# Performance work log

Hardware: AMD Instinct MI355X
Metric: run time of the kernel (lower is better)

The kernel has to match this reference:

```python
import jax, jax.numpy as jnp
import numpy as np

H, DK, OUT, IN = 8, 64, 512, 512
N, E = 30000, 100000
SQRT_DK = float(np.sqrt(DK))


def _lin_params(k, din, dout):
    kw, = jax.random.split(k, 1)
    w = jax.random.normal(kw, (din, dout), jnp.float32) * (1.0 / np.sqrt(din))
    b = jnp.zeros((dout,), jnp.float32)
    return w, b


def setup_inputs() -> dict:
    key = jax.random.key(0)
    ks = jax.random.split(key, 24)
    inp = {
        'h_paper': jax.random.normal(ks[0], (N, IN), jnp.float32),
        'h_author': jax.random.normal(ks[1], (N, IN), jnp.float32),
        'src0': jax.random.randint(ks[2], (E,), 0, N),  # author ids
        'dst0': jax.random.randint(ks[3], (E,), 0, N),  # paper ids
        'src1': jax.random.randint(ks[4], (E,), 0, N),  # paper ids
        'dst1': jax.random.randint(ks[5], (E,), 0, N),  # author ids
    }
    # per-node-type linears (type 0 = paper, type 1 = author)
    i = 6
    for t in (0, 1):
        for nm in ('Wk', 'Wq', 'Wv', 'Wa'):
            w, b = _lin_params(ks[i], IN, OUT)
            inp[f'{nm}{t}'] = w
            inp[f'b{nm[1].lower()}{t}'] = b
            i += 1
    # relation parameters (xavier ~ uniform scaled; normal approx is fine for a reference)
    inp['rel_att'] = jax.random.normal(ks[22], (2, H, DK, DK), jnp.float32) * (1.0 / np.sqrt(DK))
    inp['rel_msg'] = jax.random.normal(ks[23], (2, H, DK, DK), jnp.float32) * (1.0 / np.sqrt(DK))
    inp['rel_pri'] = jnp.ones((2, H), jnp.float32)
    inp['skip'] = jnp.ones((2,), jnp.float32)
    return inp


def _relation_agg(h_src, Wk, bk, Wv, bv, h_dst, Wq, bq, src, dst, A, M, pri):
    # project src/dst node features to multi-head k/v/q: [N, H, DK]
    k = (h_src @ Wk + bk).reshape(-1, H, DK)
    v = (h_src @ Wv + bv).reshape(-1, H, DK)
    q = (h_dst @ Wq + bq).reshape(-1, H, DK)
    # per-edge relation-specific transforms (HGT Step 1/2)
    key_e = jnp.einsum('ehk,hkd->ehd', k[src], A)   # [E,H,DK]
    val_e = jnp.einsum('ehk,hkd->ehd', v[src], M)   # [E,H,DK]
    att = (q[dst] * key_e).sum(-1) * pri / SQRT_DK  # [E,H]
    # segment softmax over incoming edges of each destination node
    m = jax.ops.segment_max(att, dst, num_segments=N)
    m = jnp.where(jnp.isfinite(m), m, 0.0)
    e = jnp.exp(att - m[dst])
    s = jax.ops.segment_sum(e, dst, num_segments=N)
    a = e / s[dst]                                   # [E,H]
    t = jax.ops.segment_sum(a[..., None] * val_e, dst, num_segments=N)
    return t.reshape(N, OUT)


def reference(h_paper, h_author, src0, dst0, src1, dst1,
              Wk0, bk0, Wq0, bq0, Wv0, bv0, Wa0, ba0,
              Wk1, bk1, Wq1, bq1, Wv1, bv1, Wa1, ba1,
              rel_att, rel_msg, rel_pri, skip):
    # relation 0: author (type 1) -> paper (type 0)
    t_paper = _relation_agg(h_author, Wk1, bk1, Wv1, bv1, h_paper, Wq0, bq0,
                            src0, dst0, rel_att[0], rel_msg[0], rel_pri[0])
    # relation 1: paper (type 0) -> author (type 1)
    t_author = _relation_agg(h_paper, Wk0, bk0, Wv0, bv0, h_author, Wq1, bq1,
                             src1, dst1, rel_att[1], rel_msg[1], rel_pri[1])
    # Step 3: target-specific aggregation with sigmoid skip (dropout=0 -> identity)
    a0 = jax.nn.sigmoid(skip[0])
    a1 = jax.nn.sigmoid(skip[1])
    out_paper = (t_paper @ Wa0 + ba0) * a0 + h_paper * (1.0 - a0)
    out_author = (t_author @ Wa1 + ba1) * a1 + h_author * (1.0 - a1)
    return jnp.stack([out_paper, out_author])  # [2, N, OUT]
```

## Files before the change

kernel.cpp:

```cpp
#include <hip/hip_runtime.h>
#include <hip/hip_bf16.h>
#include <stdint.h>

#define N_NODES 30000
#define N_PAD   30080
#define N_EDGES 100000
#define DIM     512
#define QKV_LD  1536

typedef unsigned short ushort_t;
typedef __attribute__((ext_vector_type(8))) short short8;
typedef __attribute__((ext_vector_type(8))) unsigned short ushortx8;
typedef __attribute__((ext_vector_type(4))) float floatx4;

__device__ __forceinline__ float b2f(ushort_t b) { return __uint_as_float(((unsigned)b) << 16); }
__device__ __forceinline__ ushort_t f2b(float f) {
    unsigned u = __float_as_uint(f);
    u += 0x7FFFu + ((u >> 16) & 1u);
    return (ushort_t)(u >> 16);
}

__global__ __launch_bounds__(256) void pad_copy2(const float* __restrict__ h0,
                                                 const float* __restrict__ h1,
                                                 ushort_t* __restrict__ d0,
                                                 ushort_t* __restrict__ d1) {
    const int total = N_PAD * DIM / 4;
    const int valid = N_NODES * DIM / 4;
    int idx = blockIdx.x * 256 + threadIdx.x;
    if (idx >= total) return;
    const float* s = blockIdx.y ? h1 : h0;
    ushort_t* d = blockIdx.y ? d1 : d0;
    float4 v = make_float4(0.f, 0.f, 0.f, 0.f);
    if (idx < valid) v = ((const float4*)s)[idx];
    ushort_t o[4] = {f2b(v.x), f2b(v.y), f2b(v.z), f2b(v.w)};
    ((uint2*)d)[idx] = *(const uint2*)o;
}

__global__ __launch_bounds__(256) void fuse_weights4(const float* __restrict__ Wk0, const float* __restrict__ bk0,
                                                     const float* __restrict__ Wv0, const float* __restrict__ bv0,
                                                     const float* __restrict__ Wk1, const float* __restrict__ bk1,
                                                     const float* __restrict__ Wv1, const float* __restrict__ bv1,
                                                     const float* __restrict__ rel_att, const float* __restrict__ rel_msg,
                                                     ushort_t* __restrict__ cat_p, ushort_t* __restrict__ cat_a,
                                                     float* __restrict__ bias_p, float* __restrict__ bias_a) {
    const float *W, *bvec, *A;
    ushort_t* outw; float* outb;
    switch (blockIdx.y) {
        case 0: W = Wk1; bvec = bk1; A = rel_att;          outw = cat_a + 512 * DIM;  outb = bias_a + 512;  break;
        case 1: W = Wv1; bvec = bv1; A = rel_msg;          outw = cat_a + 1024 * DIM; outb = bias_a + 1024; break;
        case 2: W = Wk0; bvec = bk0; A = rel_att + 32768;  outw = cat_p + 512 * DIM;  outb = bias_p + 512;  break;
        default: W = Wv0; bvec = bv0; A = rel_msg + 32768; outw = cat_p + 1024 * DIM; outb = bias_p + 1024; break;
    }
    int idx = blockIdx.x * 256 + threadIdx.x;
    int n = idx & 511;
    int i = idx >> 9;
    int h = n >> 6, d = n & 63;
    const float* wrow = W + i * DIM + h * 64;
    const float* acol = A + h * 4096 + d;
    float s = 0.f;
#pragma unroll 8
    for (int c = 0; c < 64; ++c) s += wrow[c] * acol[c * 64];
    outw[n * DIM + i] = f2b(s);
    if (i == 0) {
        const float* bh = bvec + h * 64;
        float sb = 0.f;
        for (int c = 0; c < 64; ++c) sb += bh[c] * acol[c * 64];
        outb[n] = sb;
    }
}

__global__ __launch_bounds__(256) void transpose4(const float* w0, const float* w1,
                                                  const float* w2, const float* w3,
                                                  ushort_t* o0, ushort_t* o1,
                                                  ushort_t* o2, ushort_t* o3) {
    const float* W; ushort_t* O;
    switch (blockIdx.y) {
        case 0: W = w0; O = o0; break;
        case 1: W = w1; O = o1; break;
        case 2: W = w2; O = o2; break;
        default: W = w3; O = o3; break;
    }
    __shared__ float tile[32][33];
    int bx = blockIdx.x & 15, by = blockIdx.x >> 4;
    int tx = threadIdx.x & 31, ty = threadIdx.x >> 5;
#pragma unroll
    for (int r = 0; r < 32; r += 8) tile[ty + r][tx] = W[(by * 32 + ty + r) * DIM + bx * 32 + tx];
    __syncthreads();
#pragma unroll
    for (int r = 0; r < 32; r += 8) O[(bx * 32 + ty + r) * DIM + by * 32 + tx] = f2b(tile[tx][ty + r]);
}

__global__ __launch_bounds__(256) void copy_biases(const float* bq0, const float* bq1,
                                                   float* bias_p, float* bias_a) {
    int i = blockIdx.x * 256 + threadIdx.x;
    bias_p[i] = bq0[i];
    bias_a[i] = bq1[i];
}

__global__ __launch_bounds__(256) void hist2(const int* __restrict__ dst0, const int* __restrict__ dst1,
                                             int* __restrict__ cnt) {
    int e = blockIdx.x * 256 + threadIdx.x;
    if (e >= 2 * N_EDGES) return;
    int rel = e >= N_EDGES;
    int d = (rel ? dst1 : dst0)[e - rel * N_EDGES];
    atomicAdd(&cnt[rel * N_NODES + d], 1);
}

__global__ __launch_bounds__(1024) void scan2(const int* __restrict__ cnt, int* __restrict__ row_ptr) {
    int rel = blockIdx.x;
    const int* c = cnt + rel * N_NODES;
    int* rp = row_ptr + rel * (N_NODES + 1);
    __shared__ int sums[1024];
    int tid = threadIdx.x;
    int base = tid * 32;
    int loc[32];
    int s = 0;
#pragma unroll
    for (int i = 0; i < 32; ++i) {
        int idx = base + i;
        int v = (idx < N_NODES) ? c[idx] : 0;
        s += v;
        loc[i] = s;
    }
    sums[tid] = s;
    __syncthreads();
    for (int off = 1; off < 1024; off <<= 1) {
        int add = (tid >= off) ? sums[tid - off] : 0;
        __syncthreads();
        sums[tid] += add;
        __syncthreads();
    }
    int pre = (tid > 0) ? sums[tid - 1] : 0;
    if (tid == 0) rp[0] = 0;
#pragma unroll
    for (int i = 0; i < 32; ++i) {
        int idx = base + i;
        if (idx < N_NODES) rp[idx + 1] = pre + loc[i];
    }
}

__global__ __launch_bounds__(256) void scatter2(const int* __restrict__ src0, const int* __restrict__ dst0,
                                                const int* __restrict__ src1, const int* __restrict__ dst1,
                                                const int* __restrict__ row_ptr,
                                                int* __restrict__ fill,
                                                int* __restrict__ colarr) {
    int e = blockIdx.x * 256 + threadIdx.x;
    if (e >= 2 * N_EDGES) return;
    int rel = e >= N_EDGES;
    int ei = e - rel * N_EDGES;
    int s = (rel ? src1 : src0)[ei];
    int d = (rel ? dst1 : dst0)[ei];
    int pos = atomicAdd(&fill[rel * N_NODES + d], 1);
    colarr[rel * N_EDGES + row_ptr[rel * (N_NODES + 1) + d] + pos] = s;
}

typedef const __attribute__((address_space(1))) unsigned int gu32;
typedef __attribute__((address_space(3))) unsigned int lu32;
__device__ __forceinline__ void gload_lds16(const void* g, void* l) {
    __builtin_amdgcn_global_load_lds((gu32*)g, (lu32*)l, 16, 0, 0);
}

__global__ __launch_bounds__(256) void gemm_proj(const ushort_t* __restrict__ Ap, const ushort_t* __restrict__ Aa,
                                                 const ushort_t* __restrict__ Bp, const ushort_t* __restrict__ Ba,
                                                 const float* __restrict__ bias_p, const float* __restrict__ bias_a,
                                                 ushort_t* __restrict__ Cp, ushort_t* __restrict__ Ca) {
    int rel = blockIdx.z;
    const ushort_t* A = rel ? Aa : Ap;
    const ushort_t* BT = rel ? Ba : Bp;
    const float* bias = rel ? bias_a : bias_p;
    ushort_t* C = rel ? Ca : Cp;

    __shared__ alignas(16) ushort_t As[128 * 32];
    __shared__ alignas(16) ushort_t Bs[128 * 32];
    int n0 = blockIdx.x * 128, m0 = blockIdx.y * 128;
    int tid = threadIdx.x;
    int w = tid >> 6, l = tid & 63;
    int wr = w >> 1, wc = w & 1;
    int fr = l & 15, fq = l >> 4;
    floatx4 acc[4][4] = {};
    const ushort_t* aF = &As[(wr * 64 + fr) * 32 + fq * 8];
    const ushort_t* bF = &Bs[(wc * 64 + fr) * 32 + fq * 8];
    int row0 = tid >> 2, c0 = (tid & 3) * 8;
    int row1 = (tid + 256) >> 2;
    int lb0 = (w * 64) * 16;
    int lb1 = (256 + w * 64) * 16;

#pragma unroll 1
    for (int kt = 0; kt < 16; ++kt) {
        int k0 = kt * 32;
        if (kt) __syncthreads();
        gload_lds16(A + (size_t)(m0 + row0) * DIM + k0 + c0, (char*)As + lb0);
        gload_lds16(BT + (size_t)(n0 + row0) * DIM + k0 + c0, (char*)Bs + lb0);
        gload_lds16(A + (size_t)(m0 + row1) * DIM + k0 + c0, (char*)As + lb1);
        gload_lds16(BT + (size_t)(n0 + row1) * DIM + k0 + c0, (char*)Bs + lb1);
        __syncthreads();
        short8 af[4], bf[4];
#pragma unroll
        for (int i = 0; i < 4; ++i) af[i] = *(const short8*)(aF + i * 16 * 32);
#pragma unroll
        for (int j = 0; j < 4; ++j) bf[j] = *(const short8*)(bF + j * 16 * 32);
#pragma unroll
        for (int i = 0; i < 4; ++i)
#pragma unroll
            for (int j = 0; j < 4; ++j)
                acc[i][j] = __builtin_amdgcn_mfma_f32_16x16x32_bf16(af[i], bf[j], acc[i][j], 0, 0, 0);
    }
#pragma unroll
    for (int i = 0; i < 4; ++i)
#pragma unroll
        for (int j = 0; j < 4; ++j) {
            int col = n0 + wc * 64 + j * 16 + fr;
            float bc = bias[col];
#pragma unroll
            for (int r = 0; r < 4; ++r) {
                int grow = m0 + wr * 64 + i * 16 + fq * 4 + r;
                C[(size_t)grow * QKV_LD + col] = f2b(acc[i][j][r] + bc);
            }
        }
}

__global__ __launch_bounds__(256) void gemm_out(const ushort_t* __restrict__ Tp, const ushort_t* __restrict__ Ta,
                                                const ushort_t* __restrict__ Wp, const ushort_t* __restrict__ Wa,
                                                const float* __restrict__ ba0, const float* __restrict__ ba1,
                                                const float* __restrict__ hp, const float* __restrict__ ha,
                                                const float* __restrict__ skipv, float* __restrict__ out) {
    int rel = blockIdx.z;
    const ushort_t* A = rel ? Ta : Tp;
    const ushort_t* BT = rel ? Wa : Wp;
    const float* bias = rel ? ba1 : ba0;
    const float* Hres = rel ? ha : hp;
    float* C = out + (size_t)rel * N_NODES * DIM;

    __shared__ alignas(16) ushort_t As[128 * 32];
    __shared__ alignas(16) ushort_t Bs[128 * 32];
    int n0 = blockIdx.x * 128, m0 = blockIdx.y * 128;
    int tid = threadIdx.x;
    int w = tid >> 6, l = tid & 63;
    int wr = w >> 1, wc = w & 1;
    int fr = l & 15, fq = l >> 4;
    floatx4 acc[4][4] = {};
    const ushort_t* aF = &As[(wr * 64 + fr) * 32 + fq * 8];
    const ushort_t* bF = &Bs[(wc * 64 + fr) * 32 + fq * 8];
    int row0 = tid >> 2, c0 = (tid & 3) * 8;
    int row1 = (tid + 256) >> 2;
    int lb0 = (w * 64) * 16;
    int lb1 = (256 + w * 64) * 16;

#pragma unroll 1
    for (int kt = 0; kt < 16; ++kt) {
        int k0 = kt * 32;
        if (kt) __syncthreads();
        gload_lds16(A + (size_t)(m0 + row0) * QKV_LD + k0 + c0, (char*)As + lb0);
        gload_lds16(BT + (size_t)(n0 + row0) * DIM + k0 + c0, (char*)Bs + lb0);
        gload_lds16(A + (size_t)(m0 + row1) * QKV_LD + k0 + c0, (char*)As + lb1);
        gload_lds16(BT + (size_t)(n0 + row1) * DIM + k0 + c0, (char*)Bs + lb1);
        __syncthreads();
        short8 af[4], bf[4];
#pragma unroll
        for (int i = 0; i < 4; ++i) af[i] = *(const short8*)(aF + i * 16 * 32);
#pragma unroll
        for (int j = 0; j < 4; ++j) bf[j] = *(const short8*)(bF + j * 16 * 32);
#pragma unroll
        for (int i = 0; i < 4; ++i)
#pragma unroll
            for (int j = 0; j < 4; ++j)
                acc[i][j] = __builtin_amdgcn_mfma_f32_16x16x32_bf16(af[i], bf[j], acc[i][j], 0, 0, 0);
    }
    float sk = skipv[rel];
    float alpha = 1.f / (1.f + __expf(-sk));
    float onem = 1.f - alpha;
#pragma unroll
    for (int i = 0; i < 4; ++i)
#pragma unroll
        for (int j = 0; j < 4; ++j) {
            int col = n0 + wc * 64 + j * 16 + fr;
            float bc = bias[col];
#pragma unroll
            for (int r = 0; r < 4; ++r) {
                int grow = m0 + wr * 64 + i * 16 + fq * 4 + r;
                if (grow < N_NODES) {
                    float v = acc[i][j][r] + bc;
                    C[(size_t)grow * DIM + col] = v * alpha + Hres[(size_t)grow * DIM + col] * onem;
                }
            }
        }
}

__global__ __launch_bounds__(256) void node_attn(const ushort_t* __restrict__ qkv_p,
                                                 ushort_t* __restrict__ qkv_p_mut,
                                                 const ushort_t* __restrict__ qkv_a,
                                                 ushort_t* __restrict__ qkv_a_mut,
                                                 const int* __restrict__ row_ptr,
                                                 const int* __restrict__ colarr,
                                                 const float* __restrict__ rel_pri) {
    int rel = blockIdx.y;
    const ushort_t* qkv_dst = rel ? qkv_a : qkv_p;
    ushort_t* t_out = rel ? qkv_a_mut : qkv_p_mut;
    const ushort_t* qkv_src = rel ? qkv_p : qkv_a;
    const int* rp = row_ptr + rel * (N_NODES + 1);
    const int* col = colarr + rel * N_EDGES;
    const float* pri = rel_pri + rel * 8;

    int w = threadIdx.x >> 6, l = threadIdx.x & 63;
    int n = blockIdx.x * 4 + w;
    float prih = pri[l >> 3] * 0.125f;

    size_t qoff = (size_t)n * QKV_LD + l * 8;
    ushortx8 qr = *(const ushortx8*)(qkv_dst + qoff);
    float qd[8];
#pragma unroll
    for (int i = 0; i < 8; ++i) qd[i] = b2f(qr[i]);

    int lo = 0, hi = 0;
    if (n < N_NODES) { lo = rp[n]; hi = rp[n + 1]; }

    float m = -3.0e38f, s = 0.f;
    float acc[8] = {};
    int j = lo;
    ushortx8 kr, vr;
    if (j < hi) {
        int sn = col[j];
        const ushort_t* kb = qkv_src + (size_t)sn * QKV_LD + 512 + l * 8;
        kr = *(const ushortx8*)kb;
        vr = *(const ushortx8*)(kb + 512);
    }
    while (j < hi) {
        ushortx8 kc = kr, vc = vr;
        ++j;
        if (j < hi) {
            int sn = col[j];
            const ushort_t* kb = qkv_src + (size_t)sn * QKV_LD + 512 + l * 8;
            kr = *(const ushortx8*)kb;
            vr = *(const ushortx8*)(kb + 512);
        }
        float dot = 0.f;
#pragma unroll
        for (int i = 0; i < 8; ++i) dot += qd[i] * b2f(kc[i]);
        dot += __shfl_xor(dot, 1);
        dot += __shfl_xor(dot, 2);
        dot += __shfl_xor(dot, 4);
        float att = dot * prih;
        float mn = fmaxf(m, att);
        float e0 = __expf(m - mn);
        float e1 = __expf(att - mn);
        s = s * e0 + e1;
#pragma unroll
        for (int i = 0; i < 8; ++i) acc[i] = acc[i] * e0 + e1 * b2f(vc[i]);
        m = mn;
    }
    float inv = (hi > lo) ? 1.f / s : 0.f;
    ushortx8 o;
#pragma unroll
    for (int i = 0; i < 8; ++i) o[i] = f2b(acc[i] * inv);
    *(ushortx8*)(t_out + qoff) = o;
}

extern "C" void kernel_launch(void* const* d_in, const int* in_sizes, int n_in,
                              void* d_out, int out_size, void* d_ws, size_t ws_size,
                              hipStream_t stream) {
    (void)in_sizes; (void)n_in; (void)out_size; (void)ws_size;
    const float* h_paper  = (const float*)d_in[0];
    const float* h_author = (const float*)d_in[1];
    const int* src0 = (const int*)d_in[2];
    const int* dst0 = (const int*)d_in[3];
    const int* src1 = (const int*)d_in[4];
    const int* dst1 = (const int*)d_in[5];
    const float* Wk0 = (const float*)d_in[6];  const float* bk0 = (const float*)d_in[7];
    const float* Wq0 = (const float*)d_in[8];  const float* bq0 = (const float*)d_in[9];
    const float* Wv0 = (const float*)d_in[10]; const float* bv0 = (const float*)d_in[11];
    const float* Wa0 = (const float*)d_in[12]; const float* ba0 = (const float*)d_in[13];
    const float* Wk1 = (const float*)d_in[14]; const float* bk1 = (const float*)d_in[15];
    const float* Wq1 = (const float*)d_in[16]; const float* bq1 = (const float*)d_in[17];
    const float* Wv1 = (const float*)d_in[18]; const float* bv1 = (const float*)d_in[19];
    const float* Wa1 = (const float*)d_in[20]; const float* ba1 = (const float*)d_in[21];
    const float* rel_att = (const float*)d_in[22];
    const float* rel_msg = (const float*)d_in[23];
    const float* rel_pri = (const float*)d_in[24];
    const float* skipv   = (const float*)d_in[25];
    float* out = (float*)d_out;

    char* p = (char*)d_ws;
    auto alloc = [&](size_t bytes) -> char* {
        char* r = p;
        p += (bytes + 255) & ~(size_t)255;
        return r;
    };
    ushort_t* hp_pad = (ushort_t*)alloc((size_t)N_PAD * DIM * 2);
    ushort_t* ha_pad = (ushort_t*)alloc((size_t)N_PAD * DIM * 2);
    ushort_t* qkv_p = (ushort_t*)alloc((size_t)N_PAD * QKV_LD * 2);
    ushort_t* qkv_a = (ushort_t*)alloc((size_t)N_PAD * QKV_LD * 2);
    ushort_t* cat_p = (ushort_t*)alloc((size_t)QKV_LD * DIM * 2);
    ushort_t* cat_a = (ushort_t*)alloc((size_t)QKV_LD * DIM * 2);
    ushort_t* WaT0 = (ushort_t*)alloc(DIM * DIM * 2);
    ushort_t* WaT1 = (ushort_t*)alloc(DIM * DIM * 2);
    float* bias_p = (float*)alloc(QKV_LD * 4);
    float* bias_a = (float*)alloc(QKV_LD * 4);
    int* cnt = (int*)alloc((size_t)4 * N_NODES * 4);
    int* fill = cnt + 2 * N_NODES;
    int* row_ptr = (int*)alloc((size_t)2 * (N_NODES + 1) * 4);
    int* colarr = (int*)alloc((size_t)2 * N_EDGES * 4);

    pad_copy2<<<dim3((N_PAD * DIM / 4 + 255) / 256, 2), 256, 0, stream>>>(h_paper, h_author, hp_pad, ha_pad);
    fuse_weights4<<<dim3(1024, 4), 256, 0, stream>>>(Wk0, bk0, Wv0, bv0, Wk1, bk1, Wv1, bv1,
                                                     rel_att, rel_msg, cat_p, cat_a, bias_p, bias_a);
    transpose4<<<dim3(256, 4), 256, 0, stream>>>(Wq0, Wq1, Wa0, Wa1, cat_p, cat_a, WaT0, WaT1);
    copy_biases<<<2, 256, 0, stream>>>(bq0, bq1, bias_p, bias_a);

    hipMemsetAsync(cnt, 0, (size_t)4 * N_NODES * 4, stream);
    hist2<<<(2 * N_EDGES + 255) / 256, 256, 0, stream>>>(dst0, dst1, cnt);
    scan2<<<2, 1024, 0, stream>>>(cnt, row_ptr);
    scatter2<<<(2 * N_EDGES + 255) / 256, 256, 0, stream>>>(src0, dst0, src1, dst1, row_ptr, fill, colarr);

    gemm_proj<<<dim3(12, 235, 2), 256, 0, stream>>>(hp_pad, ha_pad, cat_p, cat_a, bias_p, bias_a, qkv_p, qkv_a);

    node_attn<<<dim3(N_PAD / 4, 2), 256, 0, stream>>>(qkv_p, qkv_p, qkv_a, qkv_a, row_ptr, colarr, rel_pri);

    gemm_out<<<dim3(4, 235, 2), 256, 0, stream>>>(qkv_p, qkv_a, WaT0, WaT1, ba0, ba1,
                                                  h_paper, h_author, skipv, out);
}
```

Before: 692.5 us.

## Double-buffer LDS tiles in projection and output GEMMs to prefetch next K-slice

Both bf16 MFMA GEMM kernels now keep two LDS buffers per operand. Each iteration issues the global-to-LDS async loads for the next K-slice before computing on the current one, which removes one barrier per iteration and hides global load latency behind the MFMA work. Row offsets are precomputed outside the loop. The cost is twice the LDS per block (32 KB instead of 16 KB), which may lower occupancy.

```diff
diff --git a/kernel.cpp b/kernel.cpp
--- a/kernel.cpp
+++ b/kernel.cpp
@@ -170,30 +170,41 @@
     const float* bias = rel ? bias_a : bias_p;
     ushort_t* C = rel ? Ca : Cp;
 
-    __shared__ alignas(16) ushort_t As[128 * 32];
-    __shared__ alignas(16) ushort_t Bs[128 * 32];
+    __shared__ alignas(16) ushort_t As[2][128 * 32];
+    __shared__ alignas(16) ushort_t Bs[2][128 * 32];
     int n0 = blockIdx.x * 128, m0 = blockIdx.y * 128;
     int tid = threadIdx.x;
     int w = tid >> 6, l = tid & 63;
     int wr = w >> 1, wc = w & 1;
     int fr = l & 15, fq = l >> 4;
     floatx4 acc[4][4] = {};
-    const ushort_t* aF = &As[(wr * 64 + fr) * 32 + fq * 8];
-    const ushort_t* bF = &Bs[(wc * 64 + fr) * 32 + fq * 8];
     int row0 = tid >> 2, c0 = (tid & 3) * 8;
-    int row1 = (tid + 256) >> 2;
+    int row1 = row0 + 64;
     int lb0 = (w * 64) * 16;
     int lb1 = (256 + w * 64) * 16;
-
+    const size_t a0 = (size_t)(m0 + row0) * DIM + c0;
+    const size_t a1 = (size_t)(m0 + row1) * DIM + c0;
+    const size_t b0 = (size_t)(n0 + row0) * DIM + c0;
+    const size_t b1 = (size_t)(n0 + row1) * DIM + c0;
+
+    gload_lds16(A + a0, (char*)As[0] + lb0);
+    gload_lds16(BT + b0, (char*)Bs[0] + lb0);
+    gload_lds16(A + a1, (char*)As[0] + lb1);
+    gload_lds16(BT + b1, (char*)Bs[0] + lb1);
+
+    int cur = 0;
 #pragma unroll 1
     for (int kt = 0; kt < 16; ++kt) {
-        int k0 = kt * 32;
-        if (kt) __syncthreads();
-        gload_lds16(A + (size_t)(m0 + row0) * DIM + k0 + c0, (char*)As + lb0);
-        gload_lds16(BT + (size_t)(n0 + row0) * DIM + k0 + c0, (char*)Bs + lb0);
-        gload_lds16(A + (size_t)(m0 + row1) * DIM + k0 + c0, (char*)As + lb1);
-        gload_lds16(BT + (size_t)(n0 + row1) * DIM + k0 + c0, (char*)Bs + lb1);
         __syncthreads();
+        if (kt < 15) {
+            int k0 = (kt + 1) * 32;
+            gload_lds16(A + a0 + k0, (char*)As[cur ^ 1] + lb0);
+            gload_lds16(BT + b0 + k0, (char*)Bs[cur ^ 1] + lb0);
+            gload_lds16(A + a1 + k0, (char*)As[cur ^ 1] + lb1);
+            gload_lds16(BT + b1 + k0, (char*)Bs[cur ^ 1] + lb1);
+        }
+        const ushort_t* aF = &As[cur][(wr * 64 + fr) * 32 + fq * 8];
+        const ushort_t* bF = &Bs[cur][(wc * 64 + fr) * 32 + fq * 8];
         short8 af[4], bf[4];
 #pragma unroll
         for (int i = 0; i < 4; ++i) af[i] = *(const short8*)(aF + i * 16 * 32);
@@ -204,6 +215,7 @@
 #pragma unroll
             for (int j = 0; j < 4; ++j)
                 acc[i][j] = __builtin_amdgcn_mfma_f32_16x16x32_bf16(af[i], bf[j], acc[i][j], 0, 0, 0);
+        cur ^= 1;
     }
 #pragma unroll
     for (int i = 0; i < 4; ++i)
@@ -231,30 +243,41 @@
     const float* Hres = rel ? ha : hp;
     float* C = out + (size_t)rel * N_NODES * DIM;
 
-    __shared__ alignas(16) ushort_t As[128 * 32];
-    __shared__ alignas(16) ushort_t Bs[128 * 32];
+    __shared__ alignas(16) ushort_t As[2][128 * 32];
+    __shared__ alignas(16) ushort_t Bs[2][128 * 32];
     int n0 = blockIdx.x * 128, m0 = blockIdx.y * 128;
     int tid = threadIdx.x;
     int w = tid >> 6, l = tid & 63;
     int wr = w >> 1, wc = w & 1;
     int fr = l & 15, fq = l >> 4;
     floatx4 acc[4][4] = {};
-    const ushort_t* aF = &As[(wr * 64 + fr) * 32 + fq * 8];
-    const ushort_t* bF = &Bs[(wc * 64 + fr) * 32 + fq * 8];
     int row0 = tid >> 2, c0 = (tid & 3) * 8;
-    int row1 = (tid + 256) >> 2;
+    int row1 = row0 + 64;
     int lb0 = (w * 64) * 16;
     int lb1 = (256 + w * 64) * 16;
-
+    const size_t a0 = (size_t)(m0 + row0) * QKV_LD + c0;
+    const size_t a1 = (size_t)(m0 + row1) * QKV_LD + c0;
+    const size_t b0 = (size_t)(n0 + row0) * DIM + c0;
+    const size_t b1 = (size_t)(n0 + row1) * DIM + c0;
+
+    gload_lds16(A + a0, (char*)As[0] + lb0);
+    gload_lds16(BT + b0, (char*)Bs[0] + lb0);
+    gload_lds16(A + a1, (char*)As[0] + lb1);
+    gload_lds16(BT + b1, (char*)Bs[0] + lb1);
+
+    int cur = 0;
 #pragma unroll 1
     for (int kt = 0; kt < 16; ++kt) {
-        int k0 = kt * 32;
-        if (kt) __syncthreads();
-        gload_lds16(A + (size_t)(m0 + row0) * QKV_LD + k0 + c0, (char*)As + lb0);
-        gload_lds16(BT + (size_t)(n0 + row0) * DIM + k0 + c0, (char*)Bs + lb0);
-        gload_lds16(A + (size_t)(m0 + row1) * QKV_LD + k0 + c0, (char*)As + lb1);
-        gload_lds16(BT + (size_t)(n0 + row1) * DIM + k0 + c0, (char*)Bs + lb1);
         __syncthreads();
+        if (kt < 15) {
+            int k0 = (kt + 1) * 32;
+            gload_lds16(A + a0 + k0, (char*)As[cur ^ 1] + lb0);
+            gload_lds16(BT + b0 + k0, (char*)Bs[cur ^ 1] + lb0);
+            gload_lds16(A + a1 + k0, (char*)As[cur ^ 1] + lb1);
+            gload_lds16(BT + b1 + k0, (char*)Bs[cur ^ 1] + lb1);
+        }
+        const ushort_t* aF = &As[cur][(wr * 64 + fr) * 32 + fq * 8];
+        const ushort_t* bF = &Bs[cur][(wc * 64 + fr) * 32 + fq * 8];
         short8 af[4], bf[4];
 #pragma unroll
         for (int i = 0; i < 4; ++i) af[i] = *(const short8*)(aF + i * 16 * 32);
@@ -265,6 +288,7 @@
 #pragma unroll
             for (int j = 0; j < 4; ++j)
                 acc[i][j] = __builtin_amdgcn_mfma_f32_16x16x32_bf16(af[i], bf[j], acc[i][j], 0, 0, 0);
+        cur ^= 1;
     }
     float sk = skipv[rel];
     float alpha = 1.f / (1.f + __expf(-sk));
```

After: 690.0 us. No clear change (-0.4%).

## Restructure projection and output GEMMs to keep full A row-panel in LDS

Applied to the files above, without the earlier changes.

Both GEMMs now load a 64-row by full-K panel of A into padded LDS once per block, then each wave streams its own 128-column slice of B directly from global memory into registers, with no per-k-step LDS staging or barriers. The projection kernel loops over three 512-column chunks so one block covers all of QKV for its rows, and the grid becomes one block per 64-row tile per relation. This removes repeated A reloads and the per-iteration synchronisation. In exchange, B is read from global or L2 without LDS sharing, there are more accumulator registers per wave, and a large LDS footprint may reduce occupancy.

```diff
diff --git a/kernel.cpp b/kernel.cpp
--- a/kernel.cpp
+++ b/kernel.cpp
@@ -7,6 +7,7 @@
 #define N_EDGES 100000
 #define DIM     512
 #define QKV_LD  1536
+#define A_LDS_W 520
 
 typedef unsigned short ushort_t;
 typedef __attribute__((ext_vector_type(8))) short short8;
@@ -164,59 +165,57 @@
                                                  const ushort_t* __restrict__ Bp, const ushort_t* __restrict__ Ba,
                                                  const float* __restrict__ bias_p, const float* __restrict__ bias_a,
                                                  ushort_t* __restrict__ Cp, ushort_t* __restrict__ Ca) {
-    int rel = blockIdx.z;
+    int rel = blockIdx.y;
     const ushort_t* A = rel ? Aa : Ap;
     const ushort_t* BT = rel ? Ba : Bp;
     const float* bias = rel ? bias_a : bias_p;
     ushort_t* C = rel ? Ca : Cp;
 
-    __shared__ alignas(16) ushort_t As[128 * 32];
-    __shared__ alignas(16) ushort_t Bs[128 * 32];
-    int n0 = blockIdx.x * 128, m0 = blockIdx.y * 128;
+    __shared__ alignas(16) ushort_t As[64 * A_LDS_W];
+    int m0 = blockIdx.x * 64;
     int tid = threadIdx.x;
     int w = tid >> 6, l = tid & 63;
-    int wr = w >> 1, wc = w & 1;
+#pragma unroll
+    for (int t = 0; t < 16; ++t) {
+        int r = w * 16 + t;
+        gload_lds16(A + (size_t)(m0 + r) * DIM + l * 8, (char*)As + r * (A_LDS_W * 2));
+    }
     int fr = l & 15, fq = l >> 4;
-    floatx4 acc[4][4] = {};
-    const ushort_t* aF = &As[(wr * 64 + fr) * 32 + fq * 8];
-    const ushort_t* bF = &Bs[(wc * 64 + fr) * 32 + fq * 8];
-    int row0 = tid >> 2, c0 = (tid & 3) * 8;
-    int row1 = (tid + 256) >> 2;
-    int lb0 = (w * 64) * 16;
-    int lb1 = (256 + w * 64) * 16;
+    const ushort_t* aF = As + fr * A_LDS_W + fq * 8;
+    const ushort_t* Bw0 = BT + (size_t)(w * 128 + fr) * DIM + fq * 8;
+    __syncthreads();
 
 #pragma unroll 1
-    for (int kt = 0; kt < 16; ++kt) {
-        int k0 = kt * 32;
-        if (kt) __syncthreads();
-        gload_lds16(A + (size_t)(m0 + row0) * DIM + k0 + c0, (char*)As + lb0);
-        gload_lds16(BT + (size_t)(n0 + row0) * DIM + k0 + c0, (char*)Bs + lb0);
-        gload_lds16(A + (size_t)(m0 + row1) * DIM + k0 + c0, (char*)As + lb1);
-        gload_lds16(BT + (size_t)(n0 + row1) * DIM + k0 + c0, (char*)Bs + lb1);
-        __syncthreads();
-        short8 af[4], bf[4];
-#pragma unroll
-        for (int i = 0; i < 4; ++i) af[i] = *(const short8*)(aF + i * 16 * 32);
-#pragma unroll
-        for (int j = 0; j < 4; ++j) bf[j] = *(const short8*)(bF + j * 16 * 32);
-#pragma unroll
-        for (int i = 0; i < 4; ++i)
-#pragma unroll
-            for (int j = 0; j < 4; ++j)
-                acc[i][j] = __builtin_amdgcn_mfma_f32_16x16x32_bf16(af[i], bf[j], acc[i][j], 0, 0, 0);
-    }
-#pragma unroll
-    for (int i = 0; i < 4; ++i)
-#pragma unroll
-        for (int j = 0; j < 4; ++j) {
-            int col = n0 + wc * 64 + j * 16 + fr;
-            float bc = bias[col];
-#pragma unroll
-            for (int r = 0; r < 4; ++r) {
-                int grow = m0 + wr * 64 + i * 16 + fq * 4 + r;
-                C[(size_t)grow * QKV_LD + col] = f2b(acc[i][j][r] + bc);
+    for (int c = 0; c < 3; ++c) {
+        const ushort_t* Bw = Bw0 + (size_t)c * 512 * DIM;
+        floatx4 acc[4][8] = {};
+#pragma unroll 1
+        for (int kt = 0; kt < 16; ++kt) {
+            int k0 = kt * 32;
+            short8 bf[8], af[4];
+#pragma unroll
+            for (int nj = 0; nj < 8; ++nj) bf[nj] = *(const short8*)(Bw + (size_t)nj * 16 * DIM + k0);
+#pragma unroll
+            for (int mi = 0; mi < 4; ++mi) af[mi] = *(const short8*)(aF + mi * 16 * A_LDS_W + k0);
+#pragma unroll
+            for (int mi = 0; mi < 4; ++mi)
+#pragma unroll
+                for (int nj = 0; nj < 8; ++nj)
+                    acc[mi][nj] = __builtin_amdgcn_mfma_f32_16x16x32_bf16(af[mi], bf[nj], acc[mi][nj], 0, 0, 0);
+        }
+#pragma unroll
+        for (int mi = 0; mi < 4; ++mi)
+#pragma unroll
+            for (int nj = 0; nj < 8; ++nj) {
+                int col = c * 512 + w * 128 + nj * 16 + fr;
+                float bc = bias[col];
+#pragma unroll
+                for (int r = 0; r < 4; ++r) {
+                    int grow = m0 + mi * 16 + fq * 4 + r;
+                    C[(size_t)grow * QKV_LD + col] = f2b(acc[mi][nj][r] + bc);
+                }
             }
-        }
+    }
 }
 
 __global__ __launch_bounds__(256) void gemm_out(const ushort_t* __restrict__ Tp, const ushort_t* __restrict__ Ta,
@@ -224,62 +223,56 @@
                                                 const float* __restrict__ ba0, const float* __restrict__ ba1,
                                                 const float* __restrict__ hp, const float* __restrict__ ha,
                                                 const float* __restrict__ skipv, float* __restrict__ out) {
-    int rel = blockIdx.z;
+    int rel = blockIdx.y;
     const ushort_t* A = rel ? Ta : Tp;
     const ushort_t* BT = rel ? Wa : Wp;
     const float* bias = rel ? ba1 : ba0;
     const float* Hres = rel ? ha : hp;
     float* C = out + (size_t)rel * N_NODES * DIM;
 
-    __shared__ alignas(16) ushort_t As[128 * 32];
-    __shared__ alignas(16) ushort_t Bs[128 * 32];
-    int n0 = blockIdx.x * 128, m0 = blockIdx.y * 128;
+    __shared__ alignas(16) ushort_t As[64 * A_LDS_W];
+    int m0 = blockIdx.x * 64;
     int tid = threadIdx.x;
     int w = tid >> 6, l = tid & 63;
-    int wr = w >> 1, wc = w & 1;
+#pragma unroll
+    for (int t = 0; t < 16; ++t) {
+        int r = w * 16 + t;
+        gload_lds16(A + (size_t)(m0 + r) * QKV_LD + l * 8, (char*)As + r * (A_LDS_W * 2));
+    }
     int fr = l & 15, fq = l >> 4;
-    floatx4 acc[4][4] = {};
-    const ushort_t* aF = &As[(wr * 64 + fr) * 32 + fq * 8];
-    const ushort_t* bF = &Bs[(wc * 64 + fr) * 32 + fq * 8];
-    int row0 = tid >> 2, c0 = (tid & 3) * 8;
-    int row1 = (tid + 256) >> 2;
-    int lb0 = (w * 64) * 16;
-    int lb1 = (256 + w * 64) * 16;
-
+    const ushort_t* aF = As + fr * A_LDS_W + fq * 8;
+    const ushort_t* Bw = BT + (size_t)(w * 128 + fr) * DIM + fq * 8;
+    __syncthreads();
+
+    floatx4 acc[4][8] = {};
 #pragma unroll 1
     for (int kt = 0; kt < 16; ++kt) {
         int k0 = kt * 32;
-        if (kt) __syncthreads();
-        gload_lds16(A + (size_t)(m0 + row0) * QKV_LD + k0 + c0, (char*)As + lb0);
-        gload_lds16(BT + (size_t)(n0 + row0) * DIM + k0 + c0, (char*)Bs + lb0);
-        gload_lds16(A + (size_t)(m0 + row1) * QKV_LD + k0 + c0, (char*)As + lb1);
-        gload_lds16(BT + (size_t)(n0 + row1) * DIM + k0 + c0, (char*)Bs + lb1);
-        __syncthreads();
-        short8 af[4], bf[4];
-#pragma unroll
-        for (int i = 0; i < 4; ++i) af[i] = *(const short8*)(aF + i * 16 * 32);
-#pragma unroll
-        for (int j = 0; j < 4; ++j) bf[j] = *(const short8*)(bF + j * 16 * 32);
-#pragma unroll
-        for (int i = 0; i < 4; ++i)
-#pragma unroll
-            for (int j = 0; j < 4; ++j)
-                acc[i][j] = __builtin_amdgcn_mfma_f32_16x16x32_bf16(af[i], bf[j], acc[i][j], 0, 0, 0);
+        short8 bf[8], af[4];
+#pragma unroll
+        for (int nj = 0; nj < 8; ++nj) bf[nj] = *(const short8*)(Bw + (size_t)nj * 16 * DIM + k0);
+#pragma unroll
+        for (int mi = 0; mi < 4; ++mi) af[mi] = *(const short8*)(aF + mi * 16 * A_LDS_W + k0);
+#pragma unroll
+        for (int mi = 0; mi < 4; ++mi)
+#pragma unroll
+            for (int nj = 0; nj < 8; ++nj)
+                acc[mi][nj] = __builtin_amdgcn_mfma_f32_16x16x32_bf16(af[mi], bf[nj], acc[mi][nj], 0, 0, 0);
     }
     float sk = skipv[rel];
     float alpha = 1.f / (1.f + __expf(-sk));
     float onem = 1.f - alpha;
 #pragma unroll
-    for (int i = 0; i < 4; ++i)
-#pragma unroll
-        for (int j = 0; j < 4; ++j) {
-            int col = n0 + wc * 64 + j * 16 + fr;
+    for (int mi = 0; mi < 4; ++mi)
+#pragma unroll
+        for (int nj = 0; nj < 8; ++nj) {
+            int col = w * 128 + nj * 16 + fr;
             float bc = bias[col];
 #pragma unroll
             for (int r = 0; r < 4; ++r) {
-                int grow = m0 + wr * 64 + i * 16 + fq * 4 + r;
+                int grow = m0 + mi * 16 + fq * 4 + r;
                 if (grow < N_NODES) {
-                    float v = acc[i][j][r] + bc;
+                    float v = acc[mi][nj][r] + bc;
                     C[(size_t)grow * DIM + col] = v * alpha + Hres[(size_t)grow * DIM + col] * onem;
                 }
             }
@@ -411,10 +404,10 @@
     scan2<<<2, 1024, 0, stream>>>(cnt, row_ptr);
     scatter2<<<(2 * N_EDGES + 255) / 256, 256, 0, stream>>>(src0, dst0, src1, dst1, row_ptr, fill, colarr);
 
-    gemm_proj<<<dim3(12, 235, 2), 256, 0, stream>>>(hp_pad, ha_pad, cat_p, cat_a, bias_p, bias_a, qkv_p, qkv_a);
+    gemm_proj<<<dim3(N_PAD / 64, 2), 256, 0, stream>>>(hp_pad, ha_pad, cat_p, cat_a, bias_p, bias_a, qkv_p, qkv_a);
 
     node_attn<<<dim3(N_PAD / 4, 2), 256, 0, stream>>>(qkv_p, qkv_p, qkv_a, qkv_a, row_ptr, colarr, rel_pri);
 
-    gemm_out<<<dim3(4, 235, 2), 256, 0, stream>>>(qkv_p, qkv_a, WaT0, WaT1, ba0, ba1,
-                                                  h_paper, h_author, skipv, out);
-}
+    gemm_out<<<dim3(N_PAD / 64, 2), 256, 0, stream>>>(qkv_p, qkv_a, WaT0, WaT1, ba0, ba1,
+                                                      h_paper, h_author, skipv, out);
+}
```

Result: slower. 914.0 us (+32.0%).

## Use 8-wave GEMM blocks with XCD-aware linear block remapping

Applied to the files above, without the earlier changes.

Both GEMM kernels now launch 512-thread blocks (8 waves) per 128x128 tile, each wave computing a 32x64 sub-tile instead of 64x64. Half the threads stage A and half stage B, one 16-byte async load each per 64-row half. Blocks use a 1D grid remapped so consecutive blocks on the same XCD (bid&7) cover adjacent tiles, which is meant to improve L2 reuse and latency hiding. The cost is fewer accumulators per wave, so each wave does less MFMA work per LDS fragment load.

```diff
diff --git a/kernel.cpp b/kernel.cpp
--- a/kernel.cpp
+++ b/kernel.cpp
@@ -160,11 +160,15 @@
     __builtin_amdgcn_global_load_lds((gu32*)g, (lu32*)l, 16, 0, 0);
 }
 
-__global__ __launch_bounds__(256) void gemm_proj(const ushort_t* __restrict__ Ap, const ushort_t* __restrict__ Aa,
+__global__ __launch_bounds__(512) void gemm_proj(const ushort_t* __restrict__ Ap, const ushort_t* __restrict__ Aa,
                                                  const ushort_t* __restrict__ Bp, const ushort_t* __restrict__ Ba,
                                                  const float* __restrict__ bias_p, const float* __restrict__ bias_a,
                                                  ushort_t* __restrict__ Cp, ushort_t* __restrict__ Ca) {
-    int rel = blockIdx.z;
+    int bid = blockIdx.x;
+    int lin = (bid & 7) * 705 + (bid >> 3);
+    int rel = lin >= 2820;
+    int r = lin - rel * 2820;
+    int my = r / 12, nx = r - my * 12;
     const ushort_t* A = rel ? Aa : Ap;
     const ushort_t* BT = rel ? Ba : Bp;
     const float* bias = rel ? bias_a : bias_p;
@@ -172,59 +176,63 @@
 
     __shared__ alignas(16) ushort_t As[128 * 32];
     __shared__ alignas(16) ushort_t Bs[128 * 32];
-    int n0 = blockIdx.x * 128, m0 = blockIdx.y * 128;
+    int n0 = nx * 128, m0 = my * 128;
     int tid = threadIdx.x;
     int w = tid >> 6, l = tid & 63;
     int wr = w >> 1, wc = w & 1;
     int fr = l & 15, fq = l >> 4;
-    floatx4 acc[4][4] = {};
-    const ushort_t* aF = &As[(wr * 64 + fr) * 32 + fq * 8];
+    floatx4 acc[2][4] = {};
+    const ushort_t* aF = &As[(wr * 32 + fr) * 32 + fq * 8];
     const ushort_t* bF = &Bs[(wc * 64 + fr) * 32 + fq * 8];
-    int row0 = tid >> 2, c0 = (tid & 3) * 8;
-    int row1 = (tid + 256) >> 2;
-    int lb0 = (w * 64) * 16;
-    int lb1 = (256 + w * 64) * 16;
+    int g = tid & 255;
+    int srow = g >> 2, sc0 = (g & 3) * 8;
+    const ushort_t* gsrc0 = (tid < 256) ? (A + (size_t)(m0 + srow) * DIM + sc0)
+                                        : (BT + (size_t)(n0 + srow) * DIM + sc0);
+    const ushort_t* gsrc1 = gsrc0 + (size_t)64 * DIM;
+    char* ldst = (tid < 256) ? ((char*)As + g * 16) : ((char*)Bs + g * 16);
 
 #pragma unroll 1
     for (int kt = 0; kt < 16; ++kt) {
         int k0 = kt * 32;
         if (kt) __syncthreads();
-        gload_lds16(A + (size_t)(m0 + row0) * DIM + k0 + c0, (char*)As + lb0);
-        gload_lds16(BT + (size_t)(n0 + row0) * DIM + k0 + c0, (char*)Bs + lb0);
-        gload_lds16(A + (size_t)(m0 + row1) * DIM + k0 + c0, (char*)As + lb1);
-        gload_lds16(BT + (size_t)(n0 + row1) * DIM + k0 + c0, (char*)Bs + lb1);
+        gload_lds16(gsrc0 + k0, ldst);
+        gload_lds16(gsrc1 + k0, ldst + 4096);
         __syncthreads();
-        short8 af[4], bf[4];
-#pragma unroll
-        for (int i = 0; i < 4; ++i) af[i] = *(const short8*)(aF + i * 16 * 32);
+        short8 af[2], bf[4];
+#pragma unroll
+        for (int i = 0; i < 2; ++i) af[i] = *(const short8*)(aF + i * 16 * 32);
 #pragma unroll
         for (int j = 0; j < 4; ++j) bf[j] = *(const short8*)(bF + j * 16 * 32);
 #pragma unroll
-        for (int i = 0; i < 4; ++i)
+        for (int i = 0; i < 2; ++i)
 #pragma unroll
             for (int j = 0; j < 4; ++j)
                 acc[i][j] = __builtin_amdgcn_mfma_f32_16x16x32_bf16(af[i], bf[j], acc[i][j], 0, 0, 0);
     }
 #pragma unroll
-    for (int i = 0; i < 4; ++i)
+    for (int i = 0; i < 2; ++i)
 #pragma unroll
         for (int j = 0; j < 4; ++j) {
             int col = n0 + wc * 64 + j * 16 + fr;
             float bc = bias[col];
 #pragma unroll
-            for (int r = 0; r < 4; ++r) {
-                int grow = m0 + wr * 64 + i * 16 + fq * 4 + r;
-                C[(size_t)grow * QKV_LD + col] = f2b(acc[i][j][r] + bc);
+            for (int rr = 0; rr < 4; ++rr) {
+                int grow = m0 + wr * 32 + i * 16 + fq * 4 + rr;
+                C[(size_t)grow * QKV_LD + col] = f2b(acc[i][j][rr] + bc);
             }
         }
 }
 
-__global__ __launch_bounds__(256) void gemm_out(const ushort_t* __restrict__ Tp, const ushort_t* __restrict__ Ta,
+__global__ __launch_bounds__(512) void gemm_out(const ushort_t* __restrict__ Tp, const ushort_t* __restrict__ Ta,
                                                 const ushort_t* __restrict__ Wp, const ushort_t* __restrict__ Wa,
                                                 const float* __restrict__ ba0, const float* __restrict__ ba1,
                                                 const float* __restrict__ hp, const float* __restrict__ ha,
                                                 const float* __restrict__ skipv, float* __restrict__ out) {
-    int rel = blockIdx.z;
+    int bid = blockIdx.x;
+    int lin = (bid & 7) * 235 + (bid >> 3);
+    int rel = lin >= 940;
+    int r = lin - rel * 940;
+    int my = r >> 2, nx = r & 3;
     const ushort_t* A = rel ? Ta : Tp;
     const ushort_t* BT = rel ? Wa : Wp;
     const float* bias = rel ? ba1 : ba0;
@@ -233,35 +241,35 @@
 
     __shared__ alignas(16) ushort_t As[128 * 32];
     __shared__ alignas(16) ushort_t Bs[128 * 32];
-    int n0 = blockIdx.x * 128, m0 = blockIdx.y * 128;
+    int n0 = nx * 128, m0 = my * 128;
     int tid = threadIdx.x;
     int w = tid >> 6, l = tid & 63;
     int wr = w >> 1, wc = w & 1;
     int fr = l & 15, fq = l >> 4;
-    floatx4 acc[4][4] = {};
-    const ushort_t* aF = &As[(wr * 64 + fr) * 32 + fq * 8];
+    floatx4 acc[2][4] = {};
+    const ushort_t* aF = &As[(wr * 32 + fr) * 32 + fq * 8];
     const ushort_t* bF = &Bs[(wc * 64 + fr) * 32 + fq * 8];
-    int row0 = tid >> 2, c0 = (tid & 3) * 8;
-    int row1 = (tid + 256) >> 2;
-    int lb0 = (w * 64) * 16;
-    int lb1 = (256 + w * 64) * 16;
+    int g = tid & 255;
+    int srow = g >> 2, sc0 = (g & 3) * 8;
+    const ushort_t* gsrc0 = (tid < 256) ? (A + (size_t)(m0 + srow) * QKV_LD + sc0)
+                                        : (BT + (size_t)(n0 + srow) * DIM + sc0);
+    const ushort_t* gsrc1 = gsrc0 + (size_t)64 * ((tid < 256) ? QKV_LD : DIM);
+    char* ldst = (tid < 256) ? ((char*)As + g * 16) : ((char*)Bs + g * 16);
 
 #pragma unroll 1
     for (int kt = 0; kt < 16; ++kt) {
         int k0 = kt * 32;
         if (kt) __syncthreads();
-        gload_lds16(A + (size_t)(m0 + row0) * QKV_LD + k0 + c0, (char*)As + lb0);
-        gload_lds16(BT + (size_t)(n0 + row0) * DIM + k0 + c0, (char*)Bs + lb0);
-        gload_lds16(A + (size_t)(m0 + row1) * QKV_LD + k0 + c0, (char*)As + lb1);
-        gload_lds16(BT + (size_t)(n0 + row1) * DIM + k0 + c0, (char*)Bs + lb1);
+        gload_lds16(gsrc0 + k0, ldst);
+        gload_lds16(gsrc1 + k0, ldst + 4096);
         __syncthreads();
-        short8 af[4], bf[4];
-#pragma unroll
-        for (int i = 0; i < 4; ++i) af[i] = *(const short8*)(aF + i * 16 * 32);
+        short8 af[2], bf[4];
+#pragma unroll
+        for (int i = 0; i < 2; ++i) af[i] = *(const short8*)(aF + i * 16 * 32);
 #pragma unroll
         for (int j = 0; j < 4; ++j) bf[j] = *(const short8*)(bF + j * 16 * 32);
 #pragma unroll
-        for (int i = 0; i < 4; ++i)
+        for (int i = 0; i < 2; ++i)
 #pragma unroll
             for (int j = 0; j < 4; ++j)
                 acc[i][j] = __builtin_amdgcn_mfma_f32_16x16x32_bf16(af[i], bf[j], acc[i][j], 0, 0, 0);
@@ -270,16 +278,16 @@
     float alpha = 1.f / (1.f + __expf(-sk));
     float onem = 1.f - alpha;
 #pragma unroll
-    for (int i = 0; i < 4; ++i)
+    for (int i = 0; i < 2; ++i)
 #pragma unroll
         for (int j = 0; j < 4; ++j) {
             int col = n0 + wc * 64 + j * 16 + fr;
             float bc = bias[col];
 #pragma unroll
-            for (int r = 0; r < 4; ++r) {
-                int grow = m0 + wr * 64 + i * 16 + fq * 4 + r;
+            for (int rr = 0; rr < 4; ++rr) {
+                int grow = m0 + wr * 32 + i * 16 + fq * 4 + rr;
                 if (grow < N_NODES) {
-                    float v = acc[i][j][r] + bc;
+                    float v = acc[i][j][rr] + bc;
                     C[(size_t)grow * DIM + col] = v * alpha + Hres[(size_t)grow * DIM + col] * onem;
                 }
             }
@@ -411,10 +419,10 @@
     scan2<<<2, 1024, 0, stream>>>(cnt, row_ptr);
     scatter2<<<(2 * N_EDGES + 255) / 256, 256, 0, stream>>>(src0, dst0, src1, dst1, row_ptr, fill, colarr);
 
-    gemm_proj<<<dim3(12, 235, 2), 256, 0, stream>>>(hp_pad, ha_pad, cat_p, cat_a, bias_p, bias_a, qkv_p, qkv_a);
+    gemm_proj<<<5640, 512, 0, stream>>>(hp_pad, ha_pad, cat_p, cat_a, bias_p, bias_a, qkv_p, qkv_a);
 
     node_attn<<<dim3(N_PAD / 4, 2), 256, 0, stream>>>(qkv_p, qkv_p, qkv_a, qkv_a, row_ptr, colarr, rel_pri);
 
-    gemm_out<<<dim3(4, 235, 2), 256, 0, stream>>>(qkv_p, qkv_a, WaT0, WaT1, ba0, ba1,
-                                                  h_paper, h_author, skipv, out);
-}
+    gemm_out<<<1880, 512, 0, stream>>>(qkv_p, qkv_a, WaT0, WaT1, ba0, ba1,
+                                       h_paper, h_author, skipv, out);
+}
```

Measured after the change: 665.6 us. 3.9% less time.
